# Optimization experiments

Hardware: AMD Instinct MI355X
Metric: run time of the kernel (lower is better)

## Reference

```python
import jax, jax.numpy as jnp
import numpy as np

B, S, G = 128, 128, 2000          # batch, set_size, n_genes
NH, H, NLAT = 256, 4, 64          # n_hidden, n_heads, n_latent
HD = NH // H                      # head_dim = 64
NGAT = 2                          # n_gat_layers
LN_EPS = 1e-5


def _layer_norm(x, g, b):
    mu = jnp.mean(x, axis=-1, keepdims=True)
    var = jnp.var(x, axis=-1, keepdims=True)
    return (x - mu) * jax.lax.rsqrt(var + LN_EPS) * g + b


def setup_inputs() -> dict:
    key = jax.random.key(0)
    ks = jax.random.split(key, 12)
    x_set = jax.random.normal(ks[0], (B, S, G), dtype=jnp.float32)
    adj = jax.random.randint(ks[1], (B, S, S), 0, 2).astype(jnp.int32)
    # guarantee self-loops so no softmax row is fully masked
    adj = jnp.maximum(adj, jnp.eye(S, dtype=jnp.int32)[None])
    w = 0.02
    return {
        "x_set": x_set,
        "adj": adj,
        "W_in": jax.random.normal(ks[2], (G, NH), dtype=jnp.float32) * w,
        "b_in": jnp.zeros((NH,), jnp.float32),
        "ln_in_g": jnp.ones((NH,), jnp.float32),
        "ln_in_b": jnp.zeros((NH,), jnp.float32),
        "Wg": jax.random.normal(ks[3], (NGAT, NH, NH), dtype=jnp.float32) * w,
        "a_src": jax.random.normal(ks[4], (NGAT, H, HD), dtype=jnp.float32) * 0.1,
        "a_dst": jax.random.normal(ks[5], (NGAT, H, HD), dtype=jnp.float32) * 0.1,
        "a_edge": jax.random.normal(ks[6], (NGAT, H, HD), dtype=jnp.float32) * 0.1,
        "We": jax.random.normal(ks[7], (NGAT, NH, NH), dtype=jnp.float32) * w,
        "ln_g": jnp.ones((NGAT, NH), jnp.float32),
        "ln_b": jnp.zeros((NGAT, NH), jnp.float32),
        "Wz": jax.random.normal(ks[8], (NH, NLAT), dtype=jnp.float32) * w,
        "bz": jnp.zeros((NLAT,), jnp.float32),
    }


def reference(x_set, adj, W_in, b_in, ln_in_g, ln_in_b, Wg, a_src, a_dst,
              a_edge, We, ln_g, ln_b, Wz, bz):
    # input_proj: Linear -> LayerNorm -> GELU (dropout = identity in eval)
    h = jax.nn.gelu(_layer_norm(x_set @ W_in + b_in, ln_in_g, ln_in_b),
                    approximate=False)
    masked = (adj == 0)[..., None]                       # (B,S,S,1)
    for l in range(NGAT):
        hp = (h @ Wg[l]).reshape(B, S, H, HD)            # W(x) per head
        s_src = jnp.einsum('bshd,hd->bsh', hp, a_src[l])
        s_dst = jnp.einsum('bshd,hd->bsh', hp, a_dst[l])
        # edge features e_ij = h_i - h_j; edge_proj is linear (no bias), so
        # <proj(h_i - h_j), a_edge> = es_i - es_j  (exactly the original math,
        # without materializing the (B,S,S,NH) tensor)
        es = jnp.einsum('bshd,hd->bsh', (h @ We[l]).reshape(B, S, H, HD),
                        a_edge[l])
        logits = (s_src + es)[:, :, None, :] + (s_dst - es)[:, None, :, :]
        logits = jnp.where(logits >= 0, logits, 0.2 * logits)  # LeakyReLU(0.2)
        logits = jnp.where(masked, -jnp.inf, logits)
        attn = jax.nn.softmax(logits, axis=2)            # over neighbors j
        out = jnp.einsum('bijh,bjhd->bihd', attn, hp).reshape(B, S, NH)
        h = jax.nn.gelu(_layer_norm(out, ln_g[l], ln_b[l]), approximate=False)
    z_all = h @ Wz + bz                                  # (B,S,NLAT)
    return z_all
```

## Files before the change

kernel.cpp:

```cpp
#include <hip/hip_runtime.h>
#include <hip/hip_bf16.h>
#include <cstdint>
#include <cstddef>

#define BB   128
#define SS   128
#define GG   2000
#define NHID 256
#define NHEAD 4
#define HDIM 64
#define NLAT 64
#define KPAD 2048

typedef __attribute__((ext_vector_type(4))) float f32x4;
typedef __attribute__((ext_vector_type(8))) short short8;
typedef __attribute__((ext_vector_type(4))) short bfs4;
typedef __attribute__((ext_vector_type(8))) __bf16 bf8_t;

static __device__ __forceinline__ bf8_t as_bf8(short8 s){
  union { short8 s; bf8_t b; } u; u.s = s; return u.b;
}

static __device__ __forceinline__ unsigned short f2bf(float f){
  union { float f; unsigned u; } x; x.f = f;
  unsigned r = x.u + 0x7fffu + ((x.u >> 16) & 1u);
  return (unsigned short)(r >> 16);
}

#define GLOAD_LDS16(g, l) __builtin_amdgcn_global_load_lds( \
    (const __attribute__((address_space(1))) unsigned int*)(g), \
    (__attribute__((address_space(3))) unsigned int*)(l), 16, 0, 0)

__global__ __launch_bounds__(256) void k_x2bf(
    const float* __restrict__ X, unsigned short* __restrict__ Xb)
{
  const int gid = blockIdx.x * 256 + threadIdx.x;
  const int row = gid >> 8;
  const int c8  = gid & 255;
  const int k0  = c8 << 3;
  short8 v;
  if (k0 < GG) {
    f32x4 a0 = *(const f32x4*)(X + (size_t)row * GG + k0);
    f32x4 a1 = *(const f32x4*)(X + (size_t)row * GG + k0 + 4);
    v[0]=(short)f2bf(a0.x); v[1]=(short)f2bf(a0.y); v[2]=(short)f2bf(a0.z); v[3]=(short)f2bf(a0.w);
    v[4]=(short)f2bf(a1.x); v[5]=(short)f2bf(a1.y); v[6]=(short)f2bf(a1.z); v[7]=(short)f2bf(a1.w);
  } else {
#pragma unroll
    for (int t = 0; t < 8; ++t) v[t] = 0;
  }
  *(short8*)(Xb + (size_t)row * KPAD + k0) = v;
}

__global__ __launch_bounds__(256) void k_transconv(
    const float* __restrict__ W, unsigned short* __restrict__ Wt,
    int K, int N, int Kpad)
{
  int idx = blockIdx.x * 256 + threadIdx.x;
  if (idx >= N * Kpad) return;
  int n = idx / Kpad, k = idx - n * Kpad;
  float v = (k < K) ? W[(size_t)k * N + n] : 0.f;
  Wt[idx] = f2bf(v);
}

__global__ __launch_bounds__(256) void k_adjpack(
    const int* __restrict__ adj, unsigned long long* __restrict__ abits)
{
  const int wid  = blockIdx.x * 4 + (threadIdx.x >> 6);
  const int lane = threadIdx.x & 63;
  int v = adj[(size_t)wid * 64 + lane];
  unsigned long long m = __ballot(v != 0);
  if (lane == 0) abits[wid] = m;
}

__global__ __launch_bounds__(256, 2) void k_gemm2(
    const unsigned short* __restrict__ A, int lda,
    const unsigned short* __restrict__ Bt, int ldb,
    float* __restrict__ Out, unsigned short* __restrict__ Outbf,
    int nsteps, size_t psplit_stride)
{
  __shared__ __align__(16) unsigned short Ab[2][8][64][8];
  __shared__ __align__(16) unsigned short Bb[2][8][64][8];
  const int tid = threadIdx.x, l = tid & 63, w = tid >> 6;
  const int wr = w >> 1, wc = w & 1;
  const int m0 = blockIdx.x * 128, n0 = blockIdx.y * 128;
  if (Out) Out += (size_t)blockIdx.z * psplit_stride;
  const int kbase0 = blockIdx.z * nsteps * 32;

  const int rA = l & 15, kg = l >> 4;
  const unsigned short* aB = A  + (size_t)(m0 + rA) * lda + kbase0 + kg * 8;
  const unsigned short* bB = Bt + (size_t)(n0 + rA) * ldb + kbase0 + kg * 8;

  f32x4 acc[4][4];
#pragma unroll
  for (int i = 0; i < 4; ++i)
#pragma unroll
    for (int j = 0; j < 4; ++j) acc[i][j] = (f32x4)(0.f);

  auto stage = [&](int buf, int koff) {
#pragma unroll
    for (int t = 0; t < 2; ++t) {
      const int ia = 2 * w + t;
      GLOAD_LDS16(aB + (size_t)(16 * ia) * lda + koff, &Ab[buf][ia][0][0]);
      GLOAD_LDS16(bB + (size_t)(16 * ia) * ldb + koff, &Bb[buf][ia][0][0]);
    }
  };

  stage(0, 0);
  __syncthreads();

  for (int s = 0; s < nsteps; ++s) {
    const int cur = s & 1;
    if (s + 1 < nsteps) stage(cur ^ 1, (s + 1) * 32);
    short8 af[4], bfv[4];
#pragma unroll
    for (int i = 0; i < 4; ++i) af[i]  = *(const short8*)&Ab[cur][4 * wr + i][l][0];
#pragma unroll
    for (int j = 0; j < 4; ++j) bfv[j] = *(const short8*)&Bb[cur][4 * wc + j][l][0];
#pragma unroll
    for (int i = 0; i < 4; ++i)
#pragma unroll
      for (int j = 0; j < 4; ++j)
        acc[i][j] = __builtin_amdgcn_mfma_f32_16x16x32_bf16(
            as_bf8(af[i]), as_bf8(bfv[j]), acc[i][j], 0, 0, 0);
    __syncthreads();
  }

  const int orow = m0 + (wr << 6) + ((l >> 4) << 2);
  const int ocol = n0 + (wc << 6) + (l & 15);
#pragma unroll
  for (int i = 0; i < 4; ++i)
#pragma unroll
    for (int j = 0; j < 4; ++j) {
      const int row = orow + i * 16, col = ocol + j * 16;
#pragma unroll
      for (int r = 0; r < 4; ++r) {
        if (Out)   Out[(size_t)(row + r) * NHID + col] = acc[i][j][r];
        if (Outbf) Outbf[(size_t)(row + r) * NHID + col] = f2bf(acc[i][j][r]);
      }
    }
}

__global__ __launch_bounds__(256) void k_ln_fuse(
    const float* __restrict__ X0, const float* __restrict__ X1,
    const float* __restrict__ bias, const float* __restrict__ g,
    const float* __restrict__ b, unsigned short* __restrict__ out_bf,
    float* __restrict__ out_f32, const float* __restrict__ u,
    float* __restrict__ c1, float* __restrict__ c2)
{
  const int tid = threadIdx.x, l = tid & 63, w = tid >> 6;
  const f32x4 gg = *(const f32x4*)(g + l * 4);
  const f32x4 bb = *(const f32x4*)(b + l * 4);
  f32x4 bias4 = (f32x4)(0.f);
  if (bias) bias4 = *(const f32x4*)(bias + l * 4);
  f32x4 u1v[4], u2v[4];
  if (u) {
#pragma unroll
    for (int t = 0; t < 4; ++t) {
      u1v[t] = *(const f32x4*)(u + (size_t)(4 * l + t) * 4);
      u2v[t] = *(const f32x4*)(u + 1024 + (size_t)(4 * l + t) * 4);
    }
  }
  for (int it = 0; it < 4; ++it) {
    const int row = blockIdx.x * 16 + w * 4 + it;
    f32x4 x = *(const f32x4*)(X0 + (size_t)row * NHID + l * 4);
    if (X1) {
      f32x4 x1 = *(const f32x4*)(X1 + (size_t)row * NHID + l * 4);
      x.x += x1.x; x.y += x1.y; x.z += x1.z; x.w += x1.w;
    }
    x.x += bias4.x; x.y += bias4.y; x.z += bias4.z; x.w += bias4.w;
    float s  = x.x + x.y + x.z + x.w;
    float sq = x.x * x.x + x.y * x.y + x.z * x.z + x.w * x.w;
#pragma unroll
    for (int m = 1; m < 64; m <<= 1) { s += __shfl_xor(s, m); sq += __shfl_xor(sq, m); }
    const float mu   = s * (1.f / 256.f);
    const float var  = sq * (1.f / 256.f) - mu * mu;
    const float rstd = rsqrtf(var + 1e-5f);
    float y[4];
#pragma unroll
    for (int t = 0; t < 4; ++t) {
      float yy = (x[t] - mu) * rstd * gg[t] + bb[t];
      y[t] = 0.5f * yy * (1.f + erff(yy * 0.70710678118654752f));
    }
    if (out_bf) {
      bfs4 o;
#pragma unroll
      for (int t = 0; t < 4; ++t) o[t] = (short)f2bf(y[t]);
      *(bfs4*)(out_bf + (size_t)row * NHID + l * 4) = o;
    }
    if (out_f32) {
      f32x4 o; o.x = y[0]; o.y = y[1]; o.z = y[2]; o.w = y[3];
      *(f32x4*)(out_f32 + (size_t)row * NHID + l * 4) = o;
    }
    if (u) {
      float d1[4] = {0.f,0.f,0.f,0.f}, d2[4] = {0.f,0.f,0.f,0.f};
#pragma unroll
      for (int t = 0; t < 4; ++t)
#pragma unroll
        for (int h = 0; h < 4; ++h) {
          d1[h] += y[t] * u1v[t][h];
          d2[h] += y[t] * u2v[t][h];
        }
#pragma unroll
      for (int h = 0; h < 4; ++h) {
#pragma unroll
        for (int m = 1; m < 64; m <<= 1) {
          d1[h] += __shfl_xor(d1[h], m);
          d2[h] += __shfl_xor(d2[h], m);
        }
      }
      if (l == 0) {
#pragma unroll
        for (int h = 0; h < 4; ++h) {
          c1[(size_t)row * 4 + h] = d1[h];
          c2[(size_t)row * 4 + h] = d2[h];
        }
      }
    }
  }
}

__global__ __launch_bounds__(256, 1) void k_proj(
    const float* __restrict__ Wg, const float* __restrict__ We,
    const float* __restrict__ asrc, const float* __restrict__ adst,
    const float* __restrict__ aedge, float* __restrict__ u)
{
  const int lyr = blockIdx.x;
  const int k = threadIdx.x;
  const float* Wgl = Wg + (size_t)lyr * NHID * NHID;
  const float* Wel = We + (size_t)lyr * NHID * NHID;
  float* u1 = u + (size_t)lyr * 2048;
  float* u2 = u1 + 1024;
#pragma unroll
  for (int h = 0; h < 4; ++h) {
    float ss = 0.f, sd = 0.f, se = 0.f;
    const float* wg  = Wgl + k * NHID + h * 64;
    const float* we  = Wel + k * NHID + h * 64;
    const float* pas = asrc + lyr * NHEAD * HDIM + h * 64;
    const float* pad_ = adst + lyr * NHEAD * HDIM + h * 64;
    const float* pae = aedge + lyr * NHEAD * HDIM + h * 64;
#pragma unroll 4
    for (int d = 0; d < 64; ++d) {
      ss += wg[d] * pas[d];
      sd += wg[d] * pad_[d];
      se += we[d] * pae[d];
    }
    u1[k * 4 + h] = ss + se;
    u2[k * 4 + h] = sd - se;
  }
}

__global__ __launch_bounds__(256) void k_attn2(
    const unsigned short* __restrict__ hpbf, const float* __restrict__ c1,
    const float* __restrict__ c2, const unsigned long long* __restrict__ abits,
    float* __restrict__ out)
{
  __shared__ __align__(16) unsigned short Pb[4][8][64][8];
  __shared__ __align__(16) unsigned short Vb[4][4][64][8];
  __shared__ float s1[128], s2[128];
  __shared__ float mbuf[2][128], sbuf[2][128], invsum[128];
  const int head = blockIdx.x, b = blockIdx.y;
  const int tid = threadIdx.x;

  if (tid < 128) {
    const int m = b * SS + tid;
    s1[tid] = c1[m * 4 + head];
    s2[tid] = c2[m * 4 + head];
  }
  {
    const unsigned short* hb = hpbf + (size_t)b * SS * NHID + head * 64;
#pragma unroll
    for (int q = 0; q < 4; ++q) {
      const int task = tid + 256 * q;
      const int l = task & 63, tile = task >> 6;
      const int kstep = tile >> 2, nt = tile & 3;
      const int j0 = kstep * 32 + (l >> 4) * 8;
      const int d  = nt * 16 + (l & 15);
      short8 v;
#pragma unroll
      for (int e = 0; e < 8; ++e)
        v[e] = (short)hb[(size_t)(j0 + e) * NHID + d];
      *(short8*)&Vb[kstep][nt][l][0] = v;
    }
  }
  __syncthreads();

  const int i = tid & 127, half = tid >> 7;
  const float s1v = s1[i];
  const unsigned long long bits = abits[((size_t)b * SS + i) * 2 + half];

  float ma[4] = {-3.0e38f, -3.0e38f, -3.0e38f, -3.0e38f};
#pragma unroll
  for (int jl = 0; jl < 64; ++jl) {
    float x  = s1v + s2[half * 64 + jl];
    float lk = fmaxf(x, 0.2f * x);
    float xm = ((bits >> jl) & 1ull) ? lk : -3.0e38f;
    ma[jl & 3] = fmaxf(ma[jl & 3], xm);
  }
  mbuf[half][i] = fmaxf(fmaxf(ma[0], ma[1]), fmaxf(ma[2], ma[3]));
  __syncthreads();
  const float mrow = fmaxf(mbuf[0][i], mbuf[1][i]);

  float sa[4] = {0.f, 0.f, 0.f, 0.f};
#pragma unroll
  for (int grp = 0; grp < 8; ++grp) {
    short8 pv;
#pragma unroll
    for (int e = 0; e < 8; ++e) {
      const int jl = grp * 8 + e;
      float x  = s1v + s2[half * 64 + jl];
      float lk = fmaxf(x, 0.2f * x);
      float xm = ((bits >> jl) & 1ull) ? lk : -3.0e38f;
      float p  = exp2f((xm - mrow) * 1.4426950408889634f);
      sa[e & 3] += p;
      pv[e] = (short)f2bf(p);
    }
    const int j = half * 64 + grp * 8;
    const int kstep = j >> 5, g = (j >> 3) & 3;
    *(short8*)&Pb[kstep][i >> 4][(g << 4) | (i & 15)][0] = pv;
  }
  sbuf[half][i] = (sa[0] + sa[1]) + (sa[2] + sa[3]);
  __syncthreads();
  if (tid < 128) invsum[tid] = 1.f / (sbuf[0][tid] + sbuf[1][tid]);
  __syncthreads();

  const int w = tid >> 6, l = tid & 63;
  f32x4 acc[2][4];
#pragma unroll
  for (int ii = 0; ii < 2; ++ii)
#pragma unroll
    for (int nt = 0; nt < 4; ++nt) acc[ii][nt] = (f32x4)(0.f);
#pragma unroll
  for (int kstep = 0; kstep < 4; ++kstep) {
    short8 bv[4];
#pragma unroll
    for (int nt = 0; nt < 4; ++nt) bv[nt] = *(const short8*)&Vb[kstep][nt][l][0];
#pragma unroll
    for (int ii = 0; ii < 2; ++ii) {
      short8 af = *(const short8*)&Pb[kstep][2 * w + ii][l][0];
#pragma unroll
      for (int nt = 0; nt < 4; ++nt)
        acc[ii][nt] = __builtin_amdgcn_mfma_f32_16x16x32_bf16(
            as_bf8(af), as_bf8(bv[nt]), acc[ii][nt], 0, 0, 0);
    }
  }

  float* ob = out + (size_t)(b * SS) * NHID + head * 64;
#pragma unroll
  for (int ii = 0; ii < 2; ++ii) {
    const int it = 2 * w + ii;
#pragma unroll
    for (int r = 0; r < 4; ++r) {
      const int row = it * 16 + (l >> 4) * 4 + r;
      const float inv = invsum[row];
#pragma unroll
      for (int nt = 0; nt < 4; ++nt)
        ob[(size_t)row * NHID + nt * 16 + (l & 15)] = acc[ii][nt][r] * inv;
    }
  }
}

__global__ __launch_bounds__(256, 1) void k_zgemm(
    const float* __restrict__ hmat, const float* __restrict__ Wz,
    const float* __restrict__ bz, float* __restrict__ Z)
{
  __shared__ __align__(16) float hrows[64 * 256];
  const int tid = threadIdx.x, w = tid >> 6, l = tid & 63;
  const int r0 = blockIdx.x * 64;
  const f32x4* src = (const f32x4*)(hmat + (size_t)r0 * NHID);
#pragma unroll
  for (int rep = 0; rep < 16; ++rep)
    ((f32x4*)hrows)[rep * 256 + tid] = src[rep * 256 + tid];
  __syncthreads();
  const float bzv = bz[l];
  const int rbase = w * 16;
#pragma unroll
  for (int pass = 0; pass < 4; ++pass) {
    float acc0 = 0.f, acc1 = 0.f, acc2 = 0.f, acc3 = 0.f;
    const float* h0 = &hrows[(rbase + pass * 4) * 256];
#pragma unroll 8
    for (int k = 0; k < 256; ++k) {
      float wv = Wz[k * 64 + l];
      acc0 += h0[k] * wv;
      acc1 += h0[256 + k] * wv;
      acc2 += h0[512 + k] * wv;
      acc3 += h0[768 + k] * wv;
    }
    float* zp = Z + (size_t)(r0 + rbase + pass * 4) * 64 + l;
    zp[0]   = acc0 + bzv;
    zp[64]  = acc1 + bzv;
    zp[128] = acc2 + bzv;
    zp[192] = acc3 + bzv;
  }
}

extern "C" void kernel_launch(void* const* d_in, const int* in_sizes, int n_in,
                              void* d_out, int out_size, void* d_ws, size_t ws_size,
                              hipStream_t stream)
{
  const float* x_set   = (const float*)d_in[0];
  const int*   adj     = (const int*)d_in[1];
  const float* W_in    = (const float*)d_in[2];
  const float* b_in    = (const float*)d_in[3];
  const float* ln_in_g = (const float*)d_in[4];
  const float* ln_in_b = (const float*)d_in[5];
  const float* Wg      = (const float*)d_in[6];
  const float* a_src   = (const float*)d_in[7];
  const float* a_dst   = (const float*)d_in[8];
  const float* a_edge  = (const float*)d_in[9];
  const float* We      = (const float*)d_in[10];
  const float* ln_g    = (const float*)d_in[11];
  const float* ln_b    = (const float*)d_in[12];
  const float* Wz      = (const float*)d_in[13];
  const float* bz      = (const float*)d_in[14];
  float* zout = (float*)d_out;

  const int M = BB * SS;

  char* base = (char*)d_ws;
  size_t off = 0;
  auto alloc = [&](size_t bytes) { char* p = base + off; off += (bytes + 255) & ~(size_t)255; return p; };
  unsigned short* Xb    = (unsigned short*)alloc((size_t)M * KPAD * 2);
  float*          P     = (float*)alloc((size_t)M * NHID * 4 * 2);
  unsigned short* hbf   = (unsigned short*)alloc((size_t)M * NHID * 2);
  unsigned short* wt_in = (unsigned short*)alloc((size_t)NHID * KPAD * 2);
  unsigned short* wgt   = (unsigned short*)alloc((size_t)NHID * NHID * 2);
  float*          u     = (float*)alloc(2 * 2048 * 4);
  float*          c1    = (float*)alloc((size_t)M * 4 * 4);
  float*          c2    = (float*)alloc((size_t)M * 4 * 4);
  unsigned long long* abits = (unsigned long long*)alloc((size_t)BB * SS * 2 * 8);
  unsigned short* hpbf = Xb;
  float* bufA = (float*)Xb + (size_t)M * NHID;
  float* hfin = P;

  k_x2bf<<<dim3((M * (KPAD / 8)) / 256), dim3(256), 0, stream>>>(x_set, Xb);
  k_transconv<<<dim3((NHID * KPAD) / 256), dim3(256), 0, stream>>>(
      W_in, wt_in, GG, NHID, KPAD);
  k_proj<<<dim3(2), dim3(256), 0, stream>>>(Wg, We, a_src, a_dst, a_edge, u);
  k_adjpack<<<dim3(BB * SS * 2 / 4), dim3(256), 0, stream>>>(adj, abits);
  k_gemm2<<<dim3(M / 128, 2, 2), dim3(256), 0, stream>>>(
      Xb, KPAD, wt_in, KPAD, P, nullptr, 32, (size_t)M * NHID);
  k_ln_fuse<<<dim3(M / 16), dim3(256), 0, stream>>>(
      P, P + (size_t)M * NHID, b_in, ln_in_g, ln_in_b, hbf, nullptr,
      u, c1, c2);

  for (int l = 0; l < 2; ++l) {
    const float* Wgl = Wg + (size_t)l * NHID * NHID;
    k_transconv<<<dim3((NHID * NHID) / 256), dim3(256), 0, stream>>>(
        Wgl, wgt, NHID, NHID, NHID);
    k_gemm2<<<dim3(M / 128, 2, 1), dim3(256), 0, stream>>>(
        hbf, NHID, wgt, NHID, nullptr, hpbf, 8, 0);
    k_attn2<<<dim3(NHEAD, BB), dim3(256), 0, stream>>>(
        hpbf, c1, c2, abits, bufA);
    if (l == 0) {
      k_ln_fuse<<<dim3(M / 16), dim3(256), 0, stream>>>(
          bufA, nullptr, nullptr, ln_g, ln_b, hbf, nullptr,
          u + 2048, c1, c2);
    } else {
      k_ln_fuse<<<dim3(M / 16), dim3(256), 0, stream>>>(
          bufA, nullptr, nullptr, ln_g + NHID, ln_b + NHID, nullptr, hfin,
          nullptr, nullptr, nullptr);
    }
  }

  k_zgemm<<<dim3(M / 64), dim3(256), 0, stream>>>(hfin, Wz, bz, zout);
}
```

Before: 223.7 us.

## Widen input GEMM to full-N tiles and write transposed hp for attention

```diff
diff --git a/kernel.cpp b/kernel.cpp
--- a/kernel.cpp
+++ b/kernel.cpp
@@ -72,23 +72,88 @@
   if (lane == 0) abits[wid] = m;
 }
 
-__global__ __launch_bounds__(256, 2) void k_gemm2(
-    const unsigned short* __restrict__ A, int lda,
-    const unsigned short* __restrict__ Bt, int ldb,
-    float* __restrict__ Out, unsigned short* __restrict__ Outbf,
-    int nsteps, size_t psplit_stride)
+__global__ __launch_bounds__(512, 1) void k_gemm_in(
+    const unsigned short* __restrict__ A,
+    const unsigned short* __restrict__ Bt,
+    float* __restrict__ Out)
+{
+  __shared__ __align__(16) unsigned short Ab[2][8][64][8];
+  __shared__ __align__(16) unsigned short Bb[2][16][64][8];
+  const int tid = threadIdx.x, l = tid & 63, w = tid >> 6;
+  const int wr = w >> 2, wc = w & 3;
+  const int m0 = blockIdx.x * 128;
+  const int kbase0 = blockIdx.y * 1024;
+  const int nsteps = 32;
+
+  const unsigned short* aB = A  + (size_t)(m0 + (l & 15)) * KPAD + kbase0 + (l >> 4) * 8;
+  const unsigned short* bB = Bt + (size_t)(l & 15) * KPAD + kbase0 + (l >> 4) * 8;
+
+  f32x4 acc[4][4];
+#pragma unroll
+  for (int i = 0; i < 4; ++i)
+#pragma unroll
+    for (int j = 0; j < 4; ++j) acc[i][j] = (f32x4)(0.f);
+
+  auto stage = [&](int buf, int koff) {
+#pragma unroll
+    for (int q = 0; q < 3; ++q) {
+      const int tile = w * 3 + q;
+      if (tile < 8) {
+        GLOAD_LDS16(aB + (size_t)(16 * tile) * KPAD + koff, &Ab[buf][tile][0][0]);
+      } else {
+        GLOAD_LDS16(bB + (size_t)(16 * (tile - 8)) * KPAD + koff, &Bb[buf][tile - 8][0][0]);
+      }
+    }
+  };
+
+  stage(0, 0);
+  __syncthreads();
+
+  for (int s = 0; s < nsteps; ++s) {
+    const int cur = s & 1;
+    if (s + 1 < nsteps) stage(cur ^ 1, (s + 1) * 32);
+    short8 af[4], bfv[4];
+#pragma unroll
+    for (int i = 0; i < 4; ++i) af[i]  = *(const short8*)&Ab[cur][4 * wr + i][l][0];
+#pragma unroll
+    for (int j = 0; j < 4; ++j) bfv[j] = *(const short8*)&Bb[cur][4 * wc + j][l][0];
+#pragma unroll
+    for (int i = 0; i < 4; ++i)
+#pragma unroll
+      for (int j = 0; j < 4; ++j)
+        acc[i][j] = __builtin_amdgcn_mfma_f32_16x16x32_bf16(
+            as_bf8(af[i]), as_bf8(bfv[j]), acc[i][j], 0, 0, 0);
+    __syncthreads();
+  }
+
+  float* outp = Out + (size_t)blockIdx.y * ((size_t)BB * SS * NHID);
+  const int orow = m0 + (wr << 6) + ((l >> 4) << 2);
+  const int ocol = (wc << 6) + (l & 15);
+#pragma unroll
+  for (int i = 0; i < 4; ++i)
+#pragma unroll
+    for (int j = 0; j < 4; ++j) {
+      const int row = orow + i * 16, col = ocol + j * 16;
+#pragma unroll
+      for (int r = 0; r < 4; ++r)
+        outp[(size_t)(row + r) * NHID + col] = acc[i][j][r];
+    }
+}
+
+__global__ __launch_bounds__(256, 2) void k_gemm_hp(
+    const unsigned short* __restrict__ A,
+    const unsigned short* __restrict__ Bt,
+    unsigned short* __restrict__ hpT)
 {
   __shared__ __align__(16) unsigned short Ab[2][8][64][8];
   __shared__ __align__(16) unsigned short Bb[2][8][64][8];
   const int tid = threadIdx.x, l = tid & 63, w = tid >> 6;
   const int wr = w >> 1, wc = w & 1;
   const int m0 = blockIdx.x * 128, n0 = blockIdx.y * 128;
-  if (Out) Out += (size_t)blockIdx.z * psplit_stride;
-  const int kbase0 = blockIdx.z * nsteps * 32;
-
-  const int rA = l & 15, kg = l >> 4;
-  const unsigned short* aB = A  + (size_t)(m0 + rA) * lda + kbase0 + kg * 8;
-  const unsigned short* bB = Bt + (size_t)(n0 + rA) * ldb + kbase0 + kg * 8;
+
+  const int rA = l & 15;
+  const unsigned short* aB = A  + (size_t)(m0 + rA) * NHID + (l >> 4) * 8;
+  const unsigned short* bB = Bt + (size_t)(n0 + rA) * NHID + (l >> 4) * 8;
 
   f32x4 acc[4][4];
 #pragma unroll
@@ -100,17 +165,17 @@
 #pragma unroll
     for (int t = 0; t < 2; ++t) {
       const int ia = 2 * w + t;
-      GLOAD_LDS16(aB + (size_t)(16 * ia) * lda + koff, &Ab[buf][ia][0][0]);
-      GLOAD_LDS16(bB + (size_t)(16 * ia) * ldb + koff, &Bb[buf][ia][0][0]);
+      GLOAD_LDS16(aB + (size_t)(16 * ia) * NHID + koff, &Ab[buf][ia][0][0]);
+      GLOAD_LDS16(bB + (size_t)(16 * ia) * NHID + koff, &Bb[buf][ia][0][0]);
     }
   };
 
   stage(0, 0);
   __syncthreads();
 
-  for (int s = 0; s < nsteps; ++s) {
+  for (int s = 0; s < 8; ++s) {
     const int cur = s & 1;
-    if (s + 1 < nsteps) stage(cur ^ 1, (s + 1) * 32);
+    if (s + 1 < 8) stage(cur ^ 1, (s + 1) * 32);
     short8 af[4], bfv[4];
 #pragma unroll
     for (int i = 0; i < 4; ++i) af[i]  = *(const short8*)&Ab[cur][4 * wr + i][l][0];
@@ -125,18 +190,19 @@
     __syncthreads();
   }
 
-  const int orow = m0 + (wr << 6) + ((l >> 4) << 2);
+  const int bidx = m0 >> 7;
+  const int i0 = (wr << 6) + ((l >> 4) << 2);
   const int ocol = n0 + (wc << 6) + (l & 15);
+  unsigned short* hb = hpT + (size_t)bidx * NHID * SS;
 #pragma unroll
   for (int i = 0; i < 4; ++i)
 #pragma unroll
     for (int j = 0; j < 4; ++j) {
-      const int row = orow + i * 16, col = ocol + j * 16;
-#pragma unroll
-      for (int r = 0; r < 4; ++r) {
-        if (Out)   Out[(size_t)(row + r) * NHID + col] = acc[i][j][r];
-        if (Outbf) Outbf[(size_t)(row + r) * NHID + col] = f2bf(acc[i][j][r]);
-      }
+      const int col = ocol + j * 16;
+      bfs4 o;
+#pragma unroll
+      for (int r = 0; r < 4; ++r) o[r] = (short)f2bf(acc[i][j][r]);
+      *(bfs4*)&hb[(size_t)col * SS + i0 + i * 16] = o;
     }
 }
 
@@ -250,7 +316,7 @@
 }
 
 __global__ __launch_bounds__(256) void k_attn2(
-    const unsigned short* __restrict__ hpbf, const float* __restrict__ c1,
+    const unsigned short* __restrict__ hpT, const float* __restrict__ c1,
     const float* __restrict__ c2, const unsigned long long* __restrict__ abits,
     float* __restrict__ out)
 {
@@ -259,7 +325,7 @@
   __shared__ float s1[128], s2[128];
   __shared__ float mbuf[2][128], sbuf[2][128], invsum[128];
   const int head = blockIdx.x, b = blockIdx.y;
-  const int tid = threadIdx.x;
+  const int tid = threadIdx.x, w = tid >> 6, l = tid & 63;
 
   if (tid < 128) {
     const int m = b * SS + tid;
@@ -267,19 +333,14 @@
     s2[tid] = c2[m * 4 + head];
   }
   {
-    const unsigned short* hb = hpbf + (size_t)b * SS * NHID + head * 64;
+    const unsigned short* hb = hpT + ((size_t)b * NHID + head * 64) * SS;
 #pragma unroll
     for (int q = 0; q < 4; ++q) {
-      const int task = tid + 256 * q;
-      const int l = task & 63, tile = task >> 6;
+      const int tile = w * 4 + q;
       const int kstep = tile >> 2, nt = tile & 3;
-      const int j0 = kstep * 32 + (l >> 4) * 8;
-      const int d  = nt * 16 + (l & 15);
-      short8 v;
-#pragma unroll
-      for (int e = 0; e < 8; ++e)
-        v[e] = (short)hb[(size_t)(j0 + e) * NHID + d];
-      *(short8*)&Vb[kstep][nt][l][0] = v;
+      const unsigned short* src =
+          hb + (size_t)(nt * 16 + (l & 15)) * SS + kstep * 32 + (l >> 4) * 8;
+      GLOAD_LDS16(src, &Vb[kstep][nt][0][0]);
     }
   }
   __syncthreads();
@@ -323,7 +384,6 @@
   if (tid < 128) invsum[tid] = 1.f / (sbuf[0][tid] + sbuf[1][tid]);
   __syncthreads();
 
-  const int w = tid >> 6, l = tid & 63;
   f32x4 acc[2][4];
 #pragma unroll
   for (int ii = 0; ii < 2; ++ii)
@@ -428,7 +488,7 @@
   float*          c1    = (float*)alloc((size_t)M * 4 * 4);
   float*          c2    = (float*)alloc((size_t)M * 4 * 4);
   unsigned long long* abits = (unsigned long long*)alloc((size_t)BB * SS * 2 * 8);
-  unsigned short* hpbf = Xb;
+  unsigned short* hpT = Xb;
   float* bufA = (float*)Xb + (size_t)M * NHID;
   float* hfin = P;
 
@@ -437,8 +497,7 @@
       W_in, wt_in, GG, NHID, KPAD);
   k_proj<<<dim3(2), dim3(256), 0, stream>>>(Wg, We, a_src, a_dst, a_edge, u);
   k_adjpack<<<dim3(BB * SS * 2 / 4), dim3(256), 0, stream>>>(adj, abits);
-  k_gemm2<<<dim3(M / 128, 2, 2), dim3(256), 0, stream>>>(
-      Xb, KPAD, wt_in, KPAD, P, nullptr, 32, (size_t)M * NHID);
+  k_gemm_in<<<dim3(M / 128, 2), dim3(512), 0, stream>>>(Xb, wt_in, P);
   k_ln_fuse<<<dim3(M / 16), dim3(256), 0, stream>>>(
       P, P + (size_t)M * NHID, b_in, ln_in_g, ln_in_b, hbf, nullptr,
       u, c1, c2);
@@ -447,10 +506,9 @@
     const float* Wgl = Wg + (size_t)l * NHID * NHID;
     k_transconv<<<dim3((NHID * NHID) / 256), dim3(256), 0, stream>>>(
         Wgl, wgt, NHID, NHID, NHID);
-    k_gemm2<<<dim3(M / 128, 2, 1), dim3(256), 0, stream>>>(
-        hbf, NHID, wgt, NHID, nullptr, hpbf, 8, 0);
+    k_gemm_hp<<<dim3(M / 128, 2), dim3(256), 0, stream>>>(hbf, wgt, hpT);
     k_attn2<<<dim3(NHEAD, BB), dim3(256), 0, stream>>>(
-        hpbf, c1, c2, abits, bufA);
+        hpT, c1, c2, abits, bufA);
     if (l == 0) {
       k_ln_fuse<<<dim3(M / 16), dim3(256), 0, stream>>>(
           bufA, nullptr, nullptr, ln_g, ln_b, hbf, nullptr,
```

After: 230.5 us. +3.0%, slower.
